# Kernel optimization log

Hardware: AMD Instinct MI355X
Metric: run time of the kernel (lower is better)

The kernel has to match this reference:

```python
import jax, jax.numpy as jnp
import numpy as np

B, S, H, E = 32, 4096, 512, 512
NEG = -1000000000.0


def setup_inputs() -> dict:
    key = jax.random.key(0)
    ks = jax.random.split(key, 8)
    query = jax.random.normal(ks[0], (B, H), dtype=jnp.float32)
    keys = jax.random.normal(ks[1], (B, S, E), dtype=jnp.float32)
    mask = jax.random.randint(ks[2], (B, S), 0, 2, dtype=jnp.int32)
    # learned params (torch Linear: y = x @ W.T + b); store W already transposed
    Wq = jax.random.normal(ks[3], (H, H), dtype=jnp.float32) / np.sqrt(H)
    bq = jnp.zeros((H,), dtype=jnp.float32)
    Wk = jax.random.normal(ks[4], (E, H), dtype=jnp.float32) / np.sqrt(E)
    bk = jnp.zeros((H,), dtype=jnp.float32)
    v = jax.random.normal(ks[5], (H,), dtype=jnp.float32) / np.sqrt(H)
    bv = jnp.zeros((), dtype=jnp.float32)
    return {"query": query, "keys": keys, "mask": mask,
            "Wq": Wq, "bq": bq, "Wk": Wk, "bk": bk, "v": v, "bv": bv}


def reference(query, keys, mask, Wq, bq, Wk, bk, v, bv):
    # q_proj: (B, 1, H); k_proj: (B, S, H)
    q_proj = (query @ Wq + bq)[:, None, :]
    k_proj = jnp.einsum('bse,eh->bsh', keys, Wk) + bk
    # additive score: v^T tanh(q + k) + bv -> (B, S)
    scores = jnp.einsum('bsh,h->bs', jnp.tanh(q_proj + k_proj), v) + bv
    scores = jnp.where(mask == 0, NEG, scores)
    attn = jax.nn.softmax(scores, axis=-1)          # (B, S)
    context = jnp.einsum('bs,bse->be', attn, keys)  # (B, E)
    return context, attn
```

## Files before the change

### kernel.cpp

```cpp
#include <hip/hip_runtime.h>
#include <hip/hip_bf16.h>

#define BB 32
#define SS 4096
#define HH 512
#define EE 512
#define NCH 64
#define NEGV -1000000000.0f

using float4v = __attribute__((ext_vector_type(4))) float;
using short8v = __attribute__((ext_vector_type(8))) short;
using short4v = __attribute__((ext_vector_type(4))) short;

__device__ inline unsigned short f2bf(float x) {
    union { float f; unsigned int u; } c; c.f = x;
    unsigned int r = c.u + 0x7FFFu + ((c.u >> 16) & 1u);
    return (unsigned short)(r >> 16);
}
__device__ inline float bf2f(unsigned short s) {
    union { float f; unsigned int u; } c; c.u = ((unsigned int)s) << 16;
    return c.f;
}

__global__ void qproj_kernel(const float* __restrict__ query, const float* __restrict__ Wq,
                             float* __restrict__ qp) {
    __shared__ float qs[64];
    int b = blockIdx.y, e0 = blockIdx.x * 64, t = threadIdx.x;
    if (t < 64) qs[t] = query[b * HH + e0 + t];
    __syncthreads();
    int h0 = t, h1 = t + 256;
    float a0 = 0.f, a1 = 0.f;
    #pragma unroll 8
    for (int e = 0; e < 64; ++e) {
        float q = qs[e];
        a0 += q * Wq[(size_t)(e0 + e) * HH + h0];
        a1 += q * Wq[(size_t)(e0 + e) * HH + h1];
    }
    atomicAdd(&qp[b * HH + h0], a0);
    atomicAdd(&qp[b * HH + h1], a1);
}

__global__ void wkt_kernel(const float* __restrict__ Wk, unsigned short* __restrict__ WkT) {
    int g = blockIdx.x * 256 + threadIdx.x;
    int lane = g & 63, nt = (g >> 6) & 31, ks = g >> 11;
    int lq = lane >> 4, lr = lane & 15;
    int h = nt * 16 + lr;
    int e0 = ks * 32 + lq * 8;
    short8v o;
    #pragma unroll
    for (int j = 0; j < 8; ++j) o[j] = (short)f2bf(Wk[(size_t)(e0 + j) * HH + h]);
    *(short8v*)(WkT + (size_t)g * 8) = o;
}

__launch_bounds__(512, 4)
__global__ void fused_kernel(const float* __restrict__ keys, const unsigned short* __restrict__ WkT,
                             const float* __restrict__ qp, const float* __restrict__ bq,
                             const float* __restrict__ bk, const float* __restrict__ v,
                             const float* __restrict__ bv, const int* __restrict__ mask,
                             float* __restrict__ scores, float* __restrict__ part,
                             float* __restrict__ marr, float* __restrict__ larr) {
    constexpr int LDK = EE + 8;
    __shared__ unsigned short klds[64 * LDK];
    __shared__ float qp_lds[HH];
    __shared__ float v_lds[HH];
    __shared__ float red[8][64];
    __shared__ float p_lds[64];
    int b = blockIdx.y, c = blockIdx.x, s0 = c * 64;
    int tid = threadIdx.x;

    for (int i = tid; i < HH; i += 512) {
        qp_lds[i] = qp[b * HH + i] + bq[i] + bk[i];
        v_lds[i] = v[i];
    }

    const float4v* ksrc = (const float4v*)(keys + ((size_t)b * SS + s0) * EE);
    #pragma unroll
    for (int i0 = 0; i0 < 16; i0 += 4) {
        float4v kv[4];
        #pragma unroll
        for (int p = 0; p < 4; ++p) kv[p] = ksrc[tid + (i0 + p) * 512];
        #pragma unroll
        for (int p = 0; p < 4; ++p) {
            int idx = tid + (i0 + p) * 512;
            int row = idx >> 7, c4 = idx & 127;
            short4v pk;
            pk.x = (short)f2bf(kv[p].x); pk.y = (short)f2bf(kv[p].y);
            pk.z = (short)f2bf(kv[p].z); pk.w = (short)f2bf(kv[p].w);
            *(short4v*)(&klds[row * LDK + c4 * 4]) = pk;
        }
    }
    __syncthreads();

    int w = tid >> 6, lane = tid & 63;
    int lq = lane >> 4, lr = lane & 15;
    int nt0 = w * 4;

    float4v acc[4][4];
    #pragma unroll
    for (int m = 0; m < 4; ++m)
        #pragma unroll
        for (int j = 0; j < 4; ++j) acc[m][j] = (float4v){0.f, 0.f, 0.f, 0.f};

    const short8v* Wf = (const short8v*)WkT;

    #pragma unroll 2
    for (int ksg = 0; ksg < 16; ++ksg) {
        short8v bfrag[4];
        #pragma unroll
        for (int j = 0; j < 4; ++j)
            bfrag[j] = Wf[((size_t)ksg * 32 + nt0 + j) * 64 + lane];
        #pragma unroll
        for (int m = 0; m < 4; ++m) {
            short8v afrag = *(const short8v*)(&klds[(m * 16 + lr) * LDK + ksg * 32 + lq * 8]);
            #pragma unroll
            for (int j = 0; j < 4; ++j)
                acc[m][j] = __builtin_amdgcn_mfma_f32_16x16x32_bf16(afrag, bfrag[j], acc[m][j], 0, 0, 0);
        }
    }

    float part_r[4][4];
    #pragma unroll
    for (int m = 0; m < 4; ++m)
        #pragma unroll
        for (int r = 0; r < 4; ++r) part_r[m][r] = 0.f;
    #pragma unroll
    for (int j = 0; j < 4; ++j) {
        int h = (nt0 + j) * 16 + lr;
        float vj = v_lds[h], qj = qp_lds[h];
        #pragma unroll
        for (int m = 0; m < 4; ++m) {
            #pragma unroll
            for (int r = 0; r < 4; ++r) {
                float x = qj + acc[m][j][r];
                x = fminf(fmaxf(x, -12.f), 12.f);
                float e2 = __expf(2.f * x);
                part_r[m][r] += vj * ((e2 - 1.f) / (e2 + 1.f));
            }
        }
    }
    #pragma unroll
    for (int m = 0; m < 4; ++m)
        #pragma unroll
        for (int r = 0; r < 4; ++r) {
            float p = part_r[m][r];
            p += __shfl_xor(p, 1, 16);
            p += __shfl_xor(p, 2, 16);
            p += __shfl_xor(p, 4, 16);
            p += __shfl_xor(p, 8, 16);
            part_r[m][r] = p;
        }
    if (lr == 0) {
        #pragma unroll
        for (int m = 0; m < 4; ++m)
            #pragma unroll
            for (int r = 0; r < 4; ++r)
                red[w][m * 16 + lq * 4 + r] = part_r[m][r];
    }
    __syncthreads();

    if (tid < 64) {
        float sc = red[0][tid] + red[1][tid] + red[2][tid] + red[3][tid]
                 + red[4][tid] + red[5][tid] + red[6][tid] + red[7][tid] + bv[0];
        int s = s0 + tid;
        if (mask[b * SS + s] == 0) sc = NEGV;
        scores[b * SS + s] = sc;
        float mv = sc;
        #pragma unroll
        for (int off = 1; off < 64; off <<= 1) mv = fmaxf(mv, __shfl_xor(mv, off));
        float pe = __expf(sc - mv);
        float ls = pe;
        #pragma unroll
        for (int off = 1; off < 64; off <<= 1) ls += __shfl_xor(ls, off);
        p_lds[tid] = pe;
        if (tid == 0) { marr[b * NCH + c] = mv; larr[b * NCH + c] = ls; }
    }
    __syncthreads();

    float o = 0.f;
    #pragma unroll 8
    for (int s = 0; s < 64; ++s)
        o += p_lds[s] * bf2f(klds[s * LDK + tid]);
    part[((size_t)b * NCH + c) * EE + tid] = o;
}

__global__ void finalize_kernel(const float* __restrict__ scores, const float* __restrict__ part,
                                const float* __restrict__ marr, const float* __restrict__ larr,
                                float* __restrict__ ctx, float* __restrict__ attn) {
    __shared__ float wgt[NCH];
    __shared__ float Ms, Ls;
    int b = blockIdx.x, t = threadIdx.x;
    if (t < NCH) {
        float m = marr[b * NCH + t], l = larr[b * NCH + t];
        float M = m;
        #pragma unroll
        for (int off = 1; off < 64; off <<= 1) M = fmaxf(M, __shfl_xor(M, off));
        float wq = __expf(m - M);
        float L = wq * l;
        #pragma unroll
        for (int off = 1; off < 64; off <<= 1) L += __shfl_xor(L, off);
        wgt[t] = wq;
        if (t == 0) { Ms = M; Ls = L; }
    }
    __syncthreads();
    float M = Ms, invL = 1.f / Ls;
    float o = 0.f;
    #pragma unroll 8
    for (int cc = 0; cc < NCH; ++cc)
        o += wgt[cc] * part[((size_t)b * NCH + cc) * EE + t];
    ctx[b * EE + t] = o * invL;
    #pragma unroll
    for (int s = t; s < SS; s += 512)
        attn[b * SS + s] = __expf(scores[b * SS + s] - M) * invL;
}

extern "C" void kernel_launch(void* const* d_in, const int* in_sizes, int n_in,
                              void* d_out, int out_size, void* d_ws, size_t ws_size,
                              hipStream_t stream) {
    const float* query = (const float*)d_in[0];
    const float* keys  = (const float*)d_in[1];
    const int*   mask  = (const int*)d_in[2];
    const float* Wq    = (const float*)d_in[3];
    const float* bq    = (const float*)d_in[4];
    const float* Wk    = (const float*)d_in[5];
    const float* bk    = (const float*)d_in[6];
    const float* v     = (const float*)d_in[7];
    const float* bv    = (const float*)d_in[8];

    float* out  = (float*)d_out;
    float* ctx  = out;
    float* attn = out + BB * EE;

    char* ws = (char*)d_ws;
    float* qp           = (float*)ws;
    unsigned short* WkT = (unsigned short*)(ws + 65536);
    float* scores       = (float*)(ws + 589824);
    float* part         = (float*)(ws + 1114112);
    float* marr         = (float*)(ws + 5308416);
    float* larr         = (float*)(ws + 5316608);

    hipMemsetAsync(qp, 0, BB * HH * sizeof(float), stream);
    qproj_kernel<<<dim3(8, BB), 256, 0, stream>>>(query, Wq, qp);
    wkt_kernel<<<128, 256, 0, stream>>>(Wk, WkT);
    fused_kernel<<<dim3(NCH, BB), 512, 0, stream>>>(keys, WkT, qp, bq, bk, v, bv, mask,
                                                    scores, part, marr, larr);
    finalize_kernel<<<BB, 512, 0, stream>>>(scores, part, marr, larr, ctx, attn);
}
```

Baseline: 445.1 us.

## Process several chunks per 1024-thread block with register prefetch of next keys

```diff
diff --git a/kernel.cpp b/kernel.cpp
--- a/kernel.cpp
+++ b/kernel.cpp
@@ -6,11 +6,11 @@
 #define HH 512
 #define EE 512
 #define NCH 64
+#define CPB 4
 #define NEGV -1000000000.0f
 
 using float4v = __attribute__((ext_vector_type(4))) float;
 using short8v = __attribute__((ext_vector_type(8))) short;
-using short4v = __attribute__((ext_vector_type(4))) short;
 
 __device__ inline unsigned short f2bf(float x) {
     union { float f; unsigned int u; } c; c.f = x;
@@ -20,6 +20,11 @@
 __device__ inline float bf2f(unsigned short s) {
     union { float f; unsigned int u; } c; c.u = ((unsigned int)s) << 16;
     return c.f;
+}
+__device__ inline unsigned int pk2bf(float a, float b) {
+    union { __hip_bfloat162 h; unsigned int u; } c;
+    c.h = __float22bfloat162_rn(float2{a, b});
+    return c.u;
 }
 
 __global__ void qproj_kernel(const float* __restrict__ query, const float* __restrict__ Wq,
@@ -52,7 +57,7 @@
     *(short8v*)(WkT + (size_t)g * 8) = o;
 }
 
-__launch_bounds__(512, 4)
+__launch_bounds__(1024, 4)
 __global__ void fused_kernel(const float* __restrict__ keys, const unsigned short* __restrict__ WkT,
                              const float* __restrict__ qp, const float* __restrict__ bq,
                              const float* __restrict__ bk, const float* __restrict__ v,
@@ -63,124 +68,149 @@
     __shared__ unsigned short klds[64 * LDK];
     __shared__ float qp_lds[HH];
     __shared__ float v_lds[HH];
-    __shared__ float red[8][64];
+    __shared__ float red[16][64];
     __shared__ float p_lds[64];
-    int b = blockIdx.y, c = blockIdx.x, s0 = c * 64;
+    float* octx = &red[0][0];
+    int b = blockIdx.y, c0 = blockIdx.x * CPB;
     int tid = threadIdx.x;
 
-    for (int i = tid; i < HH; i += 512) {
+    for (int i = tid; i < HH; i += 1024) {
         qp_lds[i] = qp[b * HH + i] + bq[i] + bk[i];
         v_lds[i] = v[i];
     }
 
-    const float4v* ksrc = (const float4v*)(keys + ((size_t)b * SS + s0) * EE);
-    #pragma unroll
-    for (int i0 = 0; i0 < 16; i0 += 4) {
-        float4v kv[4];
-        #pragma unroll
-        for (int p = 0; p < 4; ++p) kv[p] = ksrc[tid + (i0 + p) * 512];
-        #pragma unroll
-        for (int p = 0; p < 4; ++p) {
-            int idx = tid + (i0 + p) * 512;
-            int row = idx >> 7, c4 = idx & 127;
-            short4v pk;
-            pk.x = (short)f2bf(kv[p].x); pk.y = (short)f2bf(kv[p].y);
-            pk.z = (short)f2bf(kv[p].z); pk.w = (short)f2bf(kv[p].w);
-            *(short4v*)(&klds[row * LDK + c4 * 4]) = pk;
-        }
-    }
-    __syncthreads();
-
     int w = tid >> 6, lane = tid & 63;
     int lq = lane >> 4, lr = lane & 15;
-    int nt0 = w * 4;
-
-    float4v acc[4][4];
-    #pragma unroll
-    for (int m = 0; m < 4; ++m)
-        #pragma unroll
-        for (int j = 0; j < 4; ++j) acc[m][j] = (float4v){0.f, 0.f, 0.f, 0.f};
-
+    int nt0 = w * 2;
     const short8v* Wf = (const short8v*)WkT;
 
-    #pragma unroll 2
-    for (int ksg = 0; ksg < 16; ++ksg) {
-        short8v bfrag[4];
-        #pragma unroll
-        for (int j = 0; j < 4; ++j)
-            bfrag[j] = Wf[((size_t)ksg * 32 + nt0 + j) * 64 + lane];
-        #pragma unroll
-        for (int m = 0; m < 4; ++m) {
-            short8v afrag = *(const short8v*)(&klds[(m * 16 + lr) * LDK + ksg * 32 + lq * 8]);
-            #pragma unroll
-            for (int j = 0; j < 4; ++j)
-                acc[m][j] = __builtin_amdgcn_mfma_f32_16x16x32_bf16(afrag, bfrag[j], acc[m][j], 0, 0, 0);
-        }
-    }
-
-    float part_r[4][4];
-    #pragma unroll
-    for (int m = 0; m < 4; ++m)
-        #pragma unroll
-        for (int r = 0; r < 4; ++r) part_r[m][r] = 0.f;
-    #pragma unroll
-    for (int j = 0; j < 4; ++j) {
-        int h = (nt0 + j) * 16 + lr;
-        float vj = v_lds[h], qj = qp_lds[h];
-        #pragma unroll
-        for (int m = 0; m < 4; ++m) {
+    {
+        const float4v* ksrc = (const float4v*)(keys + ((size_t)b * SS + c0 * 64) * EE);
+        float4v kv[8];
+        #pragma unroll
+        for (int p = 0; p < 8; ++p) kv[p] = ksrc[tid + p * 1024];
+        #pragma unroll
+        for (int p = 0; p < 8; ++p) {
+            int idx = tid + p * 1024, row = idx >> 7, c4 = idx & 127;
+            unsigned int u0 = pk2bf(kv[p].x, kv[p].y), u1 = pk2bf(kv[p].z, kv[p].w);
+            *(unsigned int*)(&klds[row * LDK + c4 * 4]) = u0;
+            *(unsigned int*)(&klds[row * LDK + c4 * 4 + 2]) = u1;
+        }
+    }
+    __syncthreads();
+
+    for (int i = 0; i < CPB; ++i) {
+        int c = c0 + i, s0 = c * 64;
+
+        float4v acc[4][2];
+        #pragma unroll
+        for (int m = 0; m < 4; ++m)
+            #pragma unroll
+            for (int j = 0; j < 2; ++j) acc[m][j] = (float4v){0.f, 0.f, 0.f, 0.f};
+
+        #pragma unroll 2
+        for (int ksg = 0; ksg < 16; ++ksg) {
+            short8v bfrag[2];
+            #pragma unroll
+            for (int j = 0; j < 2; ++j)
+                bfrag[j] = Wf[((size_t)ksg * 32 + nt0 + j) * 64 + lane];
+            #pragma unroll
+            for (int m = 0; m < 4; ++m) {
+                short8v afrag = *(const short8v*)(&klds[(m * 16 + lr) * LDK + ksg * 32 + lq * 8]);
+                #pragma unroll
+                for (int j = 0; j < 2; ++j)
+                    acc[m][j] = __builtin_amdgcn_mfma_f32_16x16x32_bf16(afrag, bfrag[j], acc[m][j], 0, 0, 0);
+            }
+        }
+
+        float4v kreg[8];
+        if (i < CPB - 1) {
+            const float4v* knxt = (const float4v*)(keys + ((size_t)b * SS + (c + 1) * 64) * EE);
+            #pragma unroll
+            for (int p = 0; p < 8; ++p) kreg[p] = knxt[tid + p * 1024];
+        }
+
+        float part_r[4][4];
+        #pragma unroll
+        for (int m = 0; m < 4; ++m)
+            #pragma unroll
+            for (int r = 0; r < 4; ++r) part_r[m][r] = 0.f;
+        #pragma unroll
+        for (int j = 0; j < 2; ++j) {
+            int h = (nt0 + j) * 16 + lr;
+            float vj = v_lds[h], qj = qp_lds[h], vj2 = -2.f * vj;
+            #pragma unroll
+            for (int m = 0; m < 4; ++m) {
+                #pragma unroll
+                for (int r = 0; r < 4; ++r) {
+                    float x = qj + acc[m][j][r];
+                    float rr = __frcp_rn(__expf(2.f * x) + 1.f);
+                    part_r[m][r] += __builtin_fmaf(vj2, rr, vj);
+                }
+            }
+        }
+        #pragma unroll
+        for (int m = 0; m < 4; ++m)
             #pragma unroll
             for (int r = 0; r < 4; ++r) {
-                float x = qj + acc[m][j][r];
-                x = fminf(fmaxf(x, -12.f), 12.f);
-                float e2 = __expf(2.f * x);
-                part_r[m][r] += vj * ((e2 - 1.f) / (e2 + 1.f));
-            }
-        }
-    }
-    #pragma unroll
-    for (int m = 0; m < 4; ++m)
-        #pragma unroll
-        for (int r = 0; r < 4; ++r) {
-            float p = part_r[m][r];
-            p += __shfl_xor(p, 1, 16);
-            p += __shfl_xor(p, 2, 16);
-            p += __shfl_xor(p, 4, 16);
-            p += __shfl_xor(p, 8, 16);
-            part_r[m][r] = p;
-        }
-    if (lr == 0) {
-        #pragma unroll
-        for (int m = 0; m < 4; ++m)
-            #pragma unroll
-            for (int r = 0; r < 4; ++r)
-                red[w][m * 16 + lq * 4 + r] = part_r[m][r];
-    }
-    __syncthreads();
-
-    if (tid < 64) {
-        float sc = red[0][tid] + red[1][tid] + red[2][tid] + red[3][tid]
-                 + red[4][tid] + red[5][tid] + red[6][tid] + red[7][tid] + bv[0];
-        int s = s0 + tid;
-        if (mask[b * SS + s] == 0) sc = NEGV;
-        scores[b * SS + s] = sc;
-        float mv = sc;
-        #pragma unroll
-        for (int off = 1; off < 64; off <<= 1) mv = fmaxf(mv, __shfl_xor(mv, off));
-        float pe = __expf(sc - mv);
-        float ls = pe;
-        #pragma unroll
-        for (int off = 1; off < 64; off <<= 1) ls += __shfl_xor(ls, off);
-        p_lds[tid] = pe;
-        if (tid == 0) { marr[b * NCH + c] = mv; larr[b * NCH + c] = ls; }
-    }
-    __syncthreads();
-
-    float o = 0.f;
-    #pragma unroll 8
-    for (int s = 0; s < 64; ++s)
-        o += p_lds[s] * bf2f(klds[s * LDK + tid]);
-    part[((size_t)b * NCH + c) * EE + tid] = o;
+                float p = part_r[m][r];
+                p += __shfl_xor(p, 1, 16);
+                p += __shfl_xor(p, 2, 16);
+                p += __shfl_xor(p, 4, 16);
+                p += __shfl_xor(p, 8, 16);
+                part_r[m][r] = p;
+            }
+        if (lr == 0) {
+            #pragma unroll
+            for (int m = 0; m < 4; ++m)
+                #pragma unroll
+                for (int r = 0; r < 4; ++r)
+                    red[w][m * 16 + lq * 4 + r] = part_r[m][r];
+        }
+        __syncthreads();
+
+        if (tid < 64) {
+            float sc = bv[0];
+            #pragma unroll
+            for (int ww = 0; ww < 16; ++ww) sc += red[ww][tid];
+            int s = s0 + tid;
+            if (mask[b * SS + s] == 0) sc = NEGV;
+            scores[b * SS + s] = sc;
+            float mv = sc;
+            #pragma unroll
+            for (int off = 1; off < 64; off <<= 1) mv = fmaxf(mv, __shfl_xor(mv, off));
+            float pe = __expf(sc - mv);
+            float ls = pe;
+            #pragma unroll
+            for (int off = 1; off < 64; off <<= 1) ls += __shfl_xor(ls, off);
+            p_lds[tid] = pe;
+            if (tid == 0) { marr[b * NCH + c] = mv; larr[b * NCH + c] = ls; }
+        }
+        __syncthreads();
+
+        {
+            int e = tid & 511, sh = tid >> 9;
+            float o = 0.f;
+            #pragma unroll 8
+            for (int s = sh * 32; s < sh * 32 + 32; ++s)
+                o += p_lds[s] * bf2f(klds[s * LDK + e]);
+            octx[tid] = o;
+        }
+        __syncthreads();
+        if (tid < 512)
+            part[((size_t)b * NCH + c) * EE + tid] = octx[tid] + octx[tid + 512];
+
+        if (i < CPB - 1) {
+            #pragma unroll
+            for (int p = 0; p < 8; ++p) {
+                int idx = tid + p * 1024, row = idx >> 7, c4 = idx & 127;
+                unsigned int u0 = pk2bf(kreg[p].x, kreg[p].y), u1 = pk2bf(kreg[p].z, kreg[p].w);
+                *(unsigned int*)(&klds[row * LDK + c4 * 4]) = u0;
+                *(unsigned int*)(&klds[row * LDK + c4 * 4 + 2]) = u1;
+            }
+            __syncthreads();
+        }
+    }
 }
 
 __global__ void finalize_kernel(const float* __restrict__ scores, const float* __restrict__ part,
@@ -188,7 +218,7 @@
                                 float* __restrict__ ctx, float* __restrict__ attn) {
     __shared__ float wgt[NCH];
     __shared__ float Ms, Ls;
-    int b = blockIdx.x, t = threadIdx.x;
+    int b = blockIdx.y, px = blockIdx.x, t = threadIdx.x;
     if (t < NCH) {
         float m = marr[b * NCH + t], l = larr[b * NCH + t];
         float M = m;
@@ -203,14 +233,16 @@
     }
     __syncthreads();
     float M = Ms, invL = 1.f / Ls;
-    float o = 0.f;
-    #pragma unroll 8
-    for (int cc = 0; cc < NCH; ++cc)
-        o += wgt[cc] * part[((size_t)b * NCH + cc) * EE + t];
-    ctx[b * EE + t] = o * invL;
-    #pragma unroll
-    for (int s = t; s < SS; s += 512)
-        attn[b * SS + s] = __expf(scores[b * SS + s] - M) * invL;
+    if (px == 0) {
+        float o = 0.f;
+        #pragma unroll 8
+        for (int cc = 0; cc < NCH; ++cc)
+            o += wgt[cc] * part[((size_t)b * NCH + cc) * EE + t];
+        ctx[b * EE + t] = o * invL;
+    }
+    int s0 = px * 1024;
+    attn[b * SS + s0 + t]       = __expf(scores[b * SS + s0 + t] - M) * invL;
+    attn[b * SS + s0 + t + 512] = __expf(scores[b * SS + s0 + t + 512] - M) * invL;
 }
 
 extern "C" void kernel_launch(void* const* d_in, const int* in_sizes, int n_in,
@@ -241,7 +273,7 @@
     hipMemsetAsync(qp, 0, BB * HH * sizeof(float), stream);
     qproj_kernel<<<dim3(8, BB), 256, 0, stream>>>(query, Wq, qp);
     wkt_kernel<<<128, 256, 0, stream>>>(Wk, WkT);
-    fused_kernel<<<dim3(NCH, BB), 512, 0, stream>>>(keys, WkT, qp, bq, bk, v, bv, mask,
-                                                    scores, part, marr, larr);
-    finalize_kernel<<<BB, 512, 0, stream>>>(scores, part, marr, larr, ctx, attn);
-}
+    fused_kernel<<<dim3(NCH / CPB, BB), 1024, 0, stream>>>(keys, WkT, qp, bq, bk, v, bv, mask,
+                                                           scores, part, marr, larr);
+    finalize_kernel<<<dim3(4, BB), 512, 0, stream>>>(scores, part, marr, larr, ctx, attn);
+}
```

After: 455.9 us. 1.02x slower.

## Pipeline key loads by E-quarter with MFMA and simplify tanh and finalize

Applied to the files above, without the earlier changes.

```diff
diff --git a/kernel.cpp b/kernel.cpp
--- a/kernel.cpp
+++ b/kernel.cpp
@@ -10,7 +10,15 @@
 
 using float4v = __attribute__((ext_vector_type(4))) float;
 using short8v = __attribute__((ext_vector_type(8))) short;
-using short4v = __attribute__((ext_vector_type(4))) short;
+
+#if defined(__has_builtin)
+#if __has_builtin(__builtin_amdgcn_sched_barrier)
+#define SCHED_FENCE() __builtin_amdgcn_sched_barrier(0)
+#endif
+#endif
+#ifndef SCHED_FENCE
+#define SCHED_FENCE()
+#endif
 
 __device__ inline unsigned short f2bf(float x) {
     union { float f; unsigned int u; } c; c.f = x;
@@ -20,6 +28,11 @@
 __device__ inline float bf2f(unsigned short s) {
     union { float f; unsigned int u; } c; c.u = ((unsigned int)s) << 16;
     return c.f;
+}
+__device__ inline unsigned int pk2bf(float a, float b) {
+    union { __hip_bfloat162 h; unsigned int u; } c;
+    c.h = __float22bfloat162_rn(float2{a, b});
+    return c.u;
 }
 
 __global__ void qproj_kernel(const float* __restrict__ query, const float* __restrict__ Wq,
@@ -74,20 +87,20 @@
     }
 
     const float4v* ksrc = (const float4v*)(keys + ((size_t)b * SS + s0) * EE);
-    #pragma unroll
-    for (int i0 = 0; i0 < 16; i0 += 4) {
-        float4v kv[4];
-        #pragma unroll
-        for (int p = 0; p < 4; ++p) kv[p] = ksrc[tid + (i0 + p) * 512];
-        #pragma unroll
-        for (int p = 0; p < 4; ++p) {
-            int idx = tid + (i0 + p) * 512;
-            int row = idx >> 7, c4 = idx & 127;
-            short4v pk;
-            pk.x = (short)f2bf(kv[p].x); pk.y = (short)f2bf(kv[p].y);
-            pk.z = (short)f2bf(kv[p].z); pk.w = (short)f2bf(kv[p].w);
-            *(short4v*)(&klds[row * LDK + c4 * 4]) = pk;
-        }
+    int srow = tid >> 3 << 0;
+    (void)srow;
+
+    float4v kv[4];
+    #pragma unroll
+    for (int p = 0; p < 4; ++p) {
+        int idx = tid + p * 512;
+        kv[p] = ksrc[(size_t)(idx >> 5) * 128 + (idx & 31)];
+    }
+    #pragma unroll
+    for (int p = 0; p < 4; ++p) {
+        int idx = tid + p * 512, row = idx >> 5, c4 = idx & 31;
+        *(unsigned int*)(&klds[row * LDK + c4 * 4])     = pk2bf(kv[p].x, kv[p].y);
+        *(unsigned int*)(&klds[row * LDK + c4 * 4 + 2]) = pk2bf(kv[p].z, kv[p].w);
     }
     __syncthreads();
 
@@ -103,18 +116,38 @@
 
     const short8v* Wf = (const short8v*)WkT;
 
-    #pragma unroll 2
-    for (int ksg = 0; ksg < 16; ++ksg) {
-        short8v bfrag[4];
-        #pragma unroll
-        for (int j = 0; j < 4; ++j)
-            bfrag[j] = Wf[((size_t)ksg * 32 + nt0 + j) * 64 + lane];
-        #pragma unroll
-        for (int m = 0; m < 4; ++m) {
-            short8v afrag = *(const short8v*)(&klds[(m * 16 + lr) * LDK + ksg * 32 + lq * 8]);
+    for (int q = 0; q < 4; ++q) {
+        if (q < 3) {
+            #pragma unroll
+            for (int p = 0; p < 4; ++p) {
+                int idx = tid + p * 512;
+                kv[p] = ksrc[(size_t)(idx >> 5) * 128 + (q + 1) * 32 + (idx & 31)];
+            }
+        }
+        SCHED_FENCE();
+        #pragma unroll
+        for (int ksl = 0; ksl < 4; ++ksl) {
+            int kq = q * 4 + ksl;
+            short8v bfrag[4];
             #pragma unroll
             for (int j = 0; j < 4; ++j)
-                acc[m][j] = __builtin_amdgcn_mfma_f32_16x16x32_bf16(afrag, bfrag[j], acc[m][j], 0, 0, 0);
+                bfrag[j] = Wf[((size_t)kq * 32 + nt0 + j) * 64 + lane];
+            #pragma unroll
+            for (int m = 0; m < 4; ++m) {
+                short8v afrag = *(const short8v*)(&klds[(m * 16 + lr) * LDK + kq * 32 + lq * 8]);
+                #pragma unroll
+                for (int j = 0; j < 4; ++j)
+                    acc[m][j] = __builtin_amdgcn_mfma_f32_16x16x32_bf16(afrag, bfrag[j], acc[m][j], 0, 0, 0);
+            }
+        }
+        if (q < 3) {
+            #pragma unroll
+            for (int p = 0; p < 4; ++p) {
+                int idx = tid + p * 512, row = idx >> 5, c4 = (q + 1) * 32 + (idx & 31);
+                *(unsigned int*)(&klds[row * LDK + c4 * 4])     = pk2bf(kv[p].x, kv[p].y);
+                *(unsigned int*)(&klds[row * LDK + c4 * 4 + 2]) = pk2bf(kv[p].z, kv[p].w);
+            }
+            __syncthreads();
         }
     }
 
@@ -126,15 +159,14 @@
     #pragma unroll
     for (int j = 0; j < 4; ++j) {
         int h = (nt0 + j) * 16 + lr;
-        float vj = v_lds[h], qj = qp_lds[h];
+        float vj = v_lds[h], qj = qp_lds[h], vj2 = -2.f * vj;
         #pragma unroll
         for (int m = 0; m < 4; ++m) {
             #pragma unroll
             for (int r = 0; r < 4; ++r) {
                 float x = qj + acc[m][j][r];
-                x = fminf(fmaxf(x, -12.f), 12.f);
-                float e2 = __expf(2.f * x);
-                part_r[m][r] += vj * ((e2 - 1.f) / (e2 + 1.f));
+                float rr = __frcp_rn(__expf(2.f * x) + 1.f);
+                part_r[m][r] += __builtin_fmaf(vj2, rr, vj);
             }
         }
     }
@@ -176,11 +208,15 @@
     }
     __syncthreads();
 
-    float o = 0.f;
-    #pragma unroll 8
-    for (int s = 0; s < 64; ++s)
-        o += p_lds[s] * bf2f(klds[s * LDK + tid]);
-    part[((size_t)b * NCH + c) * EE + tid] = o;
+    {
+        float o0 = 0.f, o1 = 0.f;
+        #pragma unroll 8
+        for (int s = 0; s < 32; ++s) {
+            o0 += p_lds[s]      * bf2f(klds[s * LDK + tid]);
+            o1 += p_lds[s + 32] * bf2f(klds[(s + 32) * LDK + tid]);
+        }
+        part[((size_t)b * NCH + c) * EE + tid] = o0 + o1;
+    }
 }
 
 __global__ void finalize_kernel(const float* __restrict__ scores, const float* __restrict__ part,
@@ -188,7 +224,7 @@
                                 float* __restrict__ ctx, float* __restrict__ attn) {
     __shared__ float wgt[NCH];
     __shared__ float Ms, Ls;
-    int b = blockIdx.x, t = threadIdx.x;
+    int b = blockIdx.y, px = blockIdx.x, t = threadIdx.x;
     if (t < NCH) {
         float m = marr[b * NCH + t], l = larr[b * NCH + t];
         float M = m;
@@ -203,14 +239,16 @@
     }
     __syncthreads();
     float M = Ms, invL = 1.f / Ls;
-    float o = 0.f;
-    #pragma unroll 8
-    for (int cc = 0; cc < NCH; ++cc)
-        o += wgt[cc] * part[((size_t)b * NCH + cc) * EE + t];
-    ctx[b * EE + t] = o * invL;
-    #pragma unroll
-    for (int s = t; s < SS; s += 512)
-        attn[b * SS + s] = __expf(scores[b * SS + s] - M) * invL;
+    if (px == 0) {
+        float o = 0.f;
+        #pragma unroll 8
+        for (int cc = 0; cc < NCH; ++cc)
+            o += wgt[cc] * part[((size_t)b * NCH + cc) * EE + t];
+        ctx[b * EE + t] = o * invL;
+    }
+    int s0 = px * 1024;
+    attn[b * SS + s0 + t]       = __expf(scores[b * SS + s0 + t] - M) * invL;
+    attn[b * SS + s0 + t + 512] = __expf(scores[b * SS + s0 + t + 512] - M) * invL;
 }
 
 extern "C" void kernel_launch(void* const* d_in, const int* in_sizes, int n_in,
@@ -243,5 +281,5 @@
     wkt_kernel<<<128, 256, 0, stream>>>(Wk, WkT);
     fused_kernel<<<dim3(NCH, BB), 512, 0, stream>>>(keys, WkT, qp, bq, bk, v, bv, mask,
                                                     scores, part, marr, larr);
-    finalize_kernel<<<BB, 512, 0, stream>>>(scores, part, marr, larr, ctx, attn);
-}
+    finalize_kernel<<<dim3(4, BB), 512, 0, stream>>>(scores, part, marr, larr, ctx, attn);
+}
```

Result: faster. 427.0 us (-4.1%).
